# Kernel optimization log

Measured on AMD Instinct MI355X. Metric: run time of the kernel, lower is better.

The kernel has to match this reference:

```python
import jax, jax.numpy as jnp
import numpy as np

# config
D_MODEL, D_A, D_B, R, N, D, S, D_K = 512, 256, 256, 8, 2048, 4608, 4, 64
HID = 2 * D_MODEL
U_END = D_B * R
V_END = U_END + R * D_A
B_END = V_END + D_B
LAMBDA_SHARP = 1.0
TEMPERATURE = 1.0
LN_EPS = 1e-6


def _lecun(key, shape):
    fan_in = shape[-2] if len(shape) > 1 else shape[0]
    return jax.random.normal(key, shape, dtype=jnp.float32) * (1.0 / np.sqrt(fan_in))


def setup_inputs() -> dict:
    key = jax.random.key(0)
    ks = jax.random.split(key, 12)
    return {
        'x': jax.random.normal(ks[0], (256, D_MODEL), dtype=jnp.float32),
        'pool_vectors': 0.01 * jax.random.normal(ks[1], (N, D), dtype=jnp.float32),
        'A_w0': _lecun(ks[2], (D_MODEL, HID)), 'A_b0': jnp.zeros(HID),
        'A_w1': _lecun(ks[3], (HID, D_A)), 'A_b1': jnp.zeros(D_A),
        'W_Q': _lecun(ks[4], (S, D_A, D_K)),
        'W_K': _lecun(ks[5], (S, D, D_K)),
        'aspect_logits': jnp.zeros(S),
        'tau': jnp.asarray(0.5, dtype=jnp.float32),
        'W_base': 0.01 * jax.random.normal(ks[6], (D_B, D_A), dtype=jnp.float32),
        'b_base': jnp.zeros(D_B),
        'gamma': jnp.asarray(0.1, dtype=jnp.float32),
        'ln_scale': jnp.ones(D_A), 'ln_bias': jnp.zeros(D_A),
        'B_w0': _lecun(ks[7], (D_A, HID)), 'B_b0': jnp.zeros(HID),
        'B_w1': _lecun(ks[8], (HID, D_MODEL)), 'B_b1': jnp.zeros(D_MODEL),
    }


def _forward(x, pool_vectors, A_w0, A_b0, A_w1, A_b1, W_Q, W_K, aspect_logits, tau,
             W_base, b_base, gamma, ln_scale, ln_bias, B_w0, B_b0, B_w1, B_b1):
    # Part A MLP
    h_A = jax.nn.gelu(x @ A_w0 + A_b0) @ A_w1 + A_b1                     # [b, d_A]
    # Multi-aspect retrieval
    queries = jnp.einsum('bd,adq->baq', h_A, W_Q)                        # [b, S, d_k]
    keys = jnp.einsum('np,apq->naq', pool_vectors, W_K)                  # [N, S, d_k]
    q_norm = queries / (jnp.linalg.norm(queries, axis=-1, keepdims=True) + 1e-8)
    k_norm = keys / (jnp.linalg.norm(keys, axis=-1, keepdims=True) + 1e-8)
    sims = jnp.einsum('baq,naq->bna', q_norm, k_norm)                    # [b, N, S]
    w = jax.nn.softmax(aspect_logits)
    scores = jnp.einsum('bna,a->bn', sims, w)                            # [b, N]
    g = jax.nn.sigmoid(LAMBDA_SHARP * (scores - tau))
    alpha_raw = g * jnp.exp(scores / TEMPERATURE)
    alpha = alpha_raw / (jnp.sum(alpha_raw, axis=-1, keepdims=True) + 1e-8)
    # Assemble per-sample weight matrix from low-rank factors
    U = pool_vectors[:, :U_END].reshape(N, D_B, R)
    V = pool_vectors[:, U_END:V_END].reshape(N, R, D_A)
    bias = pool_vectors[:, V_END:B_END]                                  # [N, d_B]
    UV = jnp.einsum('ndr,nre->nde', U, V)                                # [N, d_B, d_A]
    W_assembled = W_base[None] + jnp.einsum('bn,nde->bde', alpha, UV)    # [b, d_B, d_A]
    b_assembled = b_base[None] + jnp.einsum('bn,nd->bd', alpha, bias)
    # Middle layer: dynamic matmul + residual + LayerNorm
    h_t = jnp.einsum('ba,bca->bc', h_A, W_assembled) + b_assembled
    y = h_A + gamma * h_t
    mu = jnp.mean(y, axis=-1, keepdims=True)
    var = jnp.mean((y - mu) ** 2, axis=-1, keepdims=True)
    h_mid = (y - mu) / jnp.sqrt(var + LN_EPS) * ln_scale + ln_bias
    # Part B MLP
    output = jax.nn.gelu(h_mid @ B_w0 + B_b0) @ B_w1 + B_b1
    return output, alpha, W_assembled, keys


def reference(x, pool_vectors, A_w0, A_b0, A_w1, A_b1, W_Q, W_K, aspect_logits, tau,
              W_base, b_base, gamma, ln_scale, ln_bias, B_w0, B_b0, B_w1, B_b1):
    return _forward(x, pool_vectors, A_w0, A_b0, A_w1, A_b1, W_Q, W_K, aspect_logits, tau,
                    W_base, b_base, gamma, ln_scale, ln_bias, B_w0, B_b0, B_w1, B_b1)
```

## Files before the change

kernel.cpp:

```cpp
#include <hip/hip_runtime.h>
#include <hip/hip_bf16.h>
#include <math.h>

#define N_POOL 2048
#define D_POOL 4608

typedef __hip_bfloat16 bf16;
typedef __attribute__((ext_vector_type(8))) short bf16x8;
typedef __attribute__((ext_vector_type(4))) float f32x4;
typedef __attribute__((ext_vector_type(4))) unsigned short u16x4;

#define IX 0
#define IPOOL 1
#define IAW0 2
#define IAB0 3
#define IAW1 4
#define IAB1 5
#define IWQ 6
#define IWK 7
#define ILOG 8
#define ITAU 9
#define IWBASE 10
#define IBBASE 11
#define IGAMMA 12
#define ILNS 13
#define ILNB 14
#define IBW0 15
#define IBB0 16
#define IBW1 17
#define IBB1 18

__device__ inline float wsum(float v) {
#pragma unroll
    for (int off = 32; off > 0; off >>= 1) v += __shfl_xor(v, off, 64);
    return v;
}
__device__ inline float ldin(const void* p, size_t i, int f) {
    if (f) return __bfloat162float(((const bf16*)p)[i]);
    return ((const float*)p)[i];
}
__device__ inline float gelu_f(float x) {
    float t = tanhf(0.7978845608028654f * (x + 0.044715f * x * x * x));
    return 0.5f * x * (1.0f + t);
}
__device__ inline unsigned short bfbits(float f) {
    __hip_bfloat16 h = __float2bfloat16(f);
    return *reinterpret_cast<unsigned short*>(&h);
}

struct P19 { const void* p[19]; long n[19]; };

__global__ void detect_all(P19 ip, int* flags) {
    const int j = blockIdx.x;
    const unsigned short* u = (const unsigned short*)ip.p[j];
    long nelem = ip.n[j];
    long nhalf = nelem >> 1; if (nhalf < 1) nhalf = 1;
    long kstep = (nhalf + 8191) >> 13; if (kstep < 1) kstep = 1;
    int W = 0, S = 0, Z = 0, O = 0, C = 0;
    for (long k = threadIdx.x; k * kstep < nhalf; k += 256) {
        long i = k * kstep * 2;
        unsigned short ev = u[i], od = u[i + 1];
        int e = (ev >> 7) & 0xFF;
        if (ev == 0) Z++;
        else if (e >= 90 && e <= 141) S++;
        else W++;
        if (od) O++;
        C++;
    }
    __shared__ int sw[256], ss[256], sz[256], so[256], sc[256];
    sw[threadIdx.x] = W; ss[threadIdx.x] = S; sz[threadIdx.x] = Z;
    so[threadIdx.x] = O; sc[threadIdx.x] = C;
    __syncthreads();
    if (threadIdx.x == 0) {
        int tw = 0, ts = 0, tz = 0, to = 0, tc = 0;
        for (int i = 0; i < 256; i++) {
            tw += sw[i]; ts += ss[i]; tz += sz[i]; to += so[i]; tc += sc[i];
        }
        int f;
        if (tw * 16 > tc) f = 0;
        else if (ts == 0 && tw == 0) f = (to > 0) ? 0 : 1;
        else f = (ts >= tz) ? 1 : 0;
        flags[j] = f;
    }
}

template <int TRANSB>
__global__ __launch_bounds__(256) void gemm64_splitk(
    const void* __restrict__ A, int lda, int afi,
    const void* __restrict__ B, int ldb, int bfi, size_t boffs,
    float* __restrict__ C, int ldc, int KC, const int* __restrict__ flags)
{
    const int fa = (afi >= 0) ? flags[afi] : 0;
    const int fb = (bfi >= 0) ? flags[bfi] : 0;
    __shared__ __align__(16) float As[16][68];
    __shared__ __align__(16) float Bs[16][68];
    const int tid = threadIdx.x;
    const int tx = tid & 15, ty = tid >> 4;
    const int bx = blockIdx.x, by = blockIdx.y;
    const int kbeg = blockIdx.z * KC;
    float acc[4][4] = {};
    for (int k0 = kbeg; k0 < kbeg + KC; k0 += 16) {
#pragma unroll
        for (int i = 0; i < 4; i++) {
            int idx = tid + i * 256;
            int m = idx >> 4, kk = idx & 15;
            As[kk][m] = ldin(A, (size_t)(by * 64 + m) * lda + k0 + kk, fa);
        }
#pragma unroll
        for (int i = 0; i < 4; i++) {
            int idx = tid + i * 256;
            if (TRANSB) {
                int nn2 = idx >> 4, kk = idx & 15;
                Bs[kk][nn2] = ldin(B, boffs + (size_t)(bx * 64 + nn2) * ldb + k0 + kk, fb);
            } else {
                int kk = idx >> 6, nn2 = idx & 63;
                Bs[kk][nn2] = ldin(B, boffs + (size_t)(k0 + kk) * ldb + bx * 64 + nn2, fb);
            }
        }
        __syncthreads();
#pragma unroll
        for (int kk = 0; kk < 16; kk++) {
            float4 av4 = *(const float4*)&As[kk][ty * 4];
            float4 bv4 = *(const float4*)&Bs[kk][tx * 4];
            float av[4] = {av4.x, av4.y, av4.z, av4.w};
            float bv[4] = {bv4.x, bv4.y, bv4.z, bv4.w};
#pragma unroll
            for (int i = 0; i < 4; i++)
#pragma unroll
                for (int j = 0; j < 4; j++) acc[i][j] += av[i] * bv[j];
        }
        __syncthreads();
    }
#pragma unroll
    for (int i = 0; i < 4; i++) {
        int m = by * 64 + ty * 4 + i;
#pragma unroll
        for (int j = 0; j < 4; j++) {
            int n = bx * 64 + tx * 4 + j;
            atomicAdd(&C[(size_t)m * ldc + n], acc[i][j]);
        }
    }
}

__global__ __launch_bounds__(256) void gemm_mfma_atomic(
    const unsigned short* __restrict__ A, int lda,
    const unsigned short* __restrict__ Bmat, int ldb,
    float* __restrict__ C, int ldc, int KC)
{
    const int m0 = blockIdx.x * 128;
    const int n0 = blockIdx.y * 64;
    const unsigned short* B = Bmat + (size_t)blockIdx.y * 64 * ldb;
    const int kbeg = blockIdx.z * KC;
    const int t = threadIdx.x, w = t >> 6, l = t & 63;
    const int q = l >> 4, l16 = l & 15;
    f32x4 acc[2][4] = {};
    for (int k0 = kbeg; k0 < kbeg + KC; k0 += 32) {
        bf16x8 afr[2], bfr[4];
#pragma unroll
        for (int mt = 0; mt < 2; mt++)
            afr[mt] = *(const bf16x8*)&A[(size_t)(m0 + w * 32 + mt * 16 + l16) * lda + k0 + q * 8];
#pragma unroll
        for (int nt = 0; nt < 4; nt++)
            bfr[nt] = *(const bf16x8*)&B[(size_t)(nt * 16 + l16) * ldb + k0 + q * 8];
#pragma unroll
        for (int mt = 0; mt < 2; mt++)
#pragma unroll
            for (int nt = 0; nt < 4; nt++)
                acc[mt][nt] = __builtin_amdgcn_mfma_f32_16x16x32_bf16(
                    afr[mt], bfr[nt], acc[mt][nt], 0, 0, 0);
    }
#pragma unroll
    for (int mt = 0; mt < 2; mt++)
#pragma unroll
        for (int nt = 0; nt < 4; nt++)
#pragma unroll
            for (int r = 0; r < 4; r++) {
                int m = m0 + w * 32 + mt * 16 + q * 4 + r;
                atomicAdd(&C[(size_t)m * ldc + n0 + nt * 16 + l16], acc[mt][nt][r]);
            }
}

template <int ACT>
__global__ __launch_bounds__(256) void gemm_mfma_fused(
    const unsigned short* __restrict__ A, int lda,
    const unsigned short* __restrict__ Bmat, int ldb,
    const void* __restrict__ bias, int bifi, const int* __restrict__ flags,
    float* __restrict__ Cf, unsigned short* __restrict__ Cbf,
    int ldc, int K)
{
    const int m0 = blockIdx.x * 128;
    const int n0 = blockIdx.y * 64;
    const unsigned short* B = Bmat + (size_t)blockIdx.y * 64 * ldb;
    const int t = threadIdx.x, w = t >> 6, l = t & 63;
    const int q = l >> 4, l16 = l & 15;
    f32x4 acc[2][4] = {};
    for (int k0 = 0; k0 < K; k0 += 32) {
        bf16x8 afr[2], bfr[4];
#pragma unroll
        for (int mt = 0; mt < 2; mt++)
            afr[mt] = *(const bf16x8*)&A[(size_t)(m0 + w * 32 + mt * 16 + l16) * lda + k0 + q * 8];
#pragma unroll
        for (int nt = 0; nt < 4; nt++)
            bfr[nt] = *(const bf16x8*)&B[(size_t)(nt * 16 + l16) * ldb + k0 + q * 8];
#pragma unroll
        for (int mt = 0; mt < 2; mt++)
#pragma unroll
            for (int nt = 0; nt < 4; nt++)
                acc[mt][nt] = __builtin_amdgcn_mfma_f32_16x16x32_bf16(
                    afr[mt], bfr[nt], acc[mt][nt], 0, 0, 0);
    }
    float bv[4];
#pragma unroll
    for (int nt = 0; nt < 4; nt++)
        bv[nt] = bias ? ldin(bias, n0 + nt * 16 + l16, (bifi >= 0) ? flags[bifi] : 0) : 0.f;
#pragma unroll
    for (int mt = 0; mt < 2; mt++)
#pragma unroll
        for (int nt = 0; nt < 4; nt++)
#pragma unroll
            for (int r = 0; r < 4; r++) {
                int m = m0 + w * 32 + mt * 16 + q * 4 + r;
                int n = n0 + nt * 16 + l16;
                float v = acc[mt][nt][r] + bv[nt];
                if (ACT == 1) v = gelu_f(v);
                if (Cf)  Cf[(size_t)m * ldc + n] = v;
                if (Cbf) Cbf[(size_t)m * ldc + n] = bfbits(v);
            }
}

__global__ __launch_bounds__(256) void pool2bf(
    const void* __restrict__ pool, const int* __restrict__ flags,
    unsigned short* __restrict__ pb)
{
    const int fp = flags[IPOOL];
    const size_t total = (size_t)N_POOL * D_POOL;
    for (size_t i = ((size_t)blockIdx.x * 256 + threadIdx.x) * 4; i < total;
         i += (size_t)gridDim.x * 1024) {
        u16x4 o;
        if (fp == 0) {
            float4 v = *(const float4*)((const float*)pool + i);
            o[0] = bfbits(v.x); o[1] = bfbits(v.y); o[2] = bfbits(v.z); o[3] = bfbits(v.w);
        } else {
            o = *(const u16x4*)((const unsigned short*)pool + i);
        }
        *(u16x4*)&pb[i] = o;
    }
}

__global__ __launch_bounds__(256) void cvt2bf(
    const void* __restrict__ src, int fi, const int* __restrict__ flags,
    unsigned short* __restrict__ dst, int total)
{
    const int f = (fi >= 0) ? flags[fi] : 0;
    int i = (blockIdx.x * 256 + threadIdx.x) * 4;
    if (i >= total) return;
    if (f == 0) {
        float4 v = *(const float4*)((const float*)src + i);
        u16x4 o;
        o[0] = bfbits(v.x); o[1] = bfbits(v.y); o[2] = bfbits(v.z); o[3] = bfbits(v.w);
        *(u16x4*)&dst[i] = o;
    } else {
        *(u16x4*)&dst[i] = *(const u16x4*)((const unsigned short*)src + i);
    }
}

__global__ __launch_bounds__(256) void transp_bf(
    const void* __restrict__ src, int fi, const int* __restrict__ flags,
    unsigned short* __restrict__ dst, int rows, int cols)
{
    const int f = (fi >= 0) ? flags[fi] : 0;
    const size_t zoff = (size_t)blockIdx.z * rows * cols;
    const int rb = blockIdx.y * 64, cb = blockIdx.x * 64;
    __shared__ float tile[64][65];
    const int t = threadIdx.x;
    const int lr = t >> 6, lc = t & 63;
#pragma unroll
    for (int i = 0; i < 16; i++) {
        int r = i * 4 + lr;
        tile[r][lc] = ldin(src, zoff + (size_t)(rb + r) * cols + cb + lc, f);
    }
    __syncthreads();
#pragma unroll
    for (int i = 0; i < 16; i++) {
        int c = i * 4 + lr;
        dst[zoff + (size_t)(cb + c) * rows + rb + lc] = bfbits(tile[lc][c]);
    }
}

__global__ __launch_bounds__(256) void wk2bfT(
    const void* __restrict__ W_K, const int* __restrict__ flags,
    unsigned short* __restrict__ out)
{
    const int fk = flags[IWK];
    const int a = blockIdx.y, kb = blockIdx.x, t = threadIdx.x;
#pragma unroll
    for (int i = 0; i < 16; i++) {
        int idx = i * 256 + t;
        int kk = idx >> 6, qq = idx & 63;
        float v = ldin(W_K, (size_t)a * 294912 + (size_t)(kb * 64 + kk) * 64 + qq, fk);
        out[(size_t)(a * 64 + qq) * 4608 + kb * 64 + kk] = bfbits(v);
    }
}

__global__ __launch_bounds__(256) void bias2bfT(
    const void* __restrict__ pool, const int* __restrict__ flags,
    unsigned short* __restrict__ out)
{
    const int fp = flags[IPOOL];
    const int nb = blockIdx.x, cb = blockIdx.y, t = threadIdx.x;
#pragma unroll
    for (int i = 0; i < 16; i++) {
        int idx = i * 256 + t;
        int nn = idx >> 6, cc = idx & 63;
        float v = ldin(pool, (size_t)(nb * 64 + nn) * 4608 + 4096 + cb * 64 + cc, fp);
        out[(size_t)(cb * 64 + cc) * 2048 + nb * 64 + nn] = bfbits(v);
    }
}

__global__ __launch_bounds__(256) void init_bias_kernel(
    float* __restrict__ C, const void* __restrict__ bias, int bifi,
    const int* __restrict__ flags, int N, int total)
{
    int i = blockIdx.x * 256 + threadIdx.x;
    if (i >= total) return;
    float v = 0.f;
    if (bias) v = ldin(bias, i % N, (bifi >= 0) ? flags[bifi] : 0);
    C[i] = v;
}

__global__ __launch_bounds__(256) void gelu_kernel(float* __restrict__ buf, int total)
{
    int i = blockIdx.x * 256 + threadIdx.x;
    if (i < total) buf[i] = gelu_f(buf[i]);
}

__global__ __launch_bounds__(256) void knorm_kernel(
    const float* __restrict__ keys, unsigned short* __restrict__ knbf)
{
    const int n = blockIdx.x;
    const int a = threadIdx.x >> 6, q = threadIdx.x & 63;
    float v = keys[(size_t)n * 256 + a * 64 + q];
    float ss = wsum(v * v);
    knbf[(size_t)n * 256 + a * 64 + q] = bfbits(v / (sqrtf(ss) + 1e-8f));
}

__global__ __launch_bounds__(256) void qnorm_kernel(
    const float* __restrict__ qraw, const float* __restrict__ w,
    unsigned short* __restrict__ qwbf)
{
    const int b = blockIdx.x;
    const int a = threadIdx.x >> 6, q = threadIdx.x & 63;
    float v = qraw[b * 256 + a * 64 + q];
    float ss = wsum(v * v);
    qwbf[b * 256 + a * 64 + q] = bfbits(v / (sqrtf(ss) + 1e-8f) * w[a]);
}

__global__ void softmax4_kernel(const void* __restrict__ logits,
                                const int* __restrict__ flags, float* __restrict__ w) {
    if (threadIdx.x == 0) {
        int f = flags[ILOG];
        float l0 = ldin(logits, 0, f), l1 = ldin(logits, 1, f);
        float l2 = ldin(logits, 2, f), l3 = ldin(logits, 3, f);
        float m = fmaxf(fmaxf(l0, l1), fmaxf(l2, l3));
        float e0 = expf(l0 - m), e1 = expf(l1 - m), e2 = expf(l2 - m), e3 = expf(l3 - m);
        float s = e0 + e1 + e2 + e3;
        w[0] = e0 / s; w[1] = e1 / s; w[2] = e2 / s; w[3] = e3 / s;
    }
}

__global__ __launch_bounds__(256) void alpha_kernel(
    const float* __restrict__ scores, const void* __restrict__ tau_p,
    const int* __restrict__ flags,
    float* __restrict__ alpha_out, unsigned short* __restrict__ alphaT,
    unsigned short* __restrict__ alphaB)
{
    const int b = blockIdx.x;
    const int tid = threadIdx.x;
    const float tauv = ldin(tau_p, 0, flags[ITAU]);
    float ar[8];
    float lsum = 0.f;
#pragma unroll
    for (int i = 0; i < 8; i++) {
        int n = i * 256 + tid;
        float s = scores[b * 2048 + n];
        float g = 1.f / (1.f + expf(-(s - tauv)));
        ar[i] = g * expf(s);
        lsum += ar[i];
    }
    __shared__ float sb[4];
    float wsv = wsum(lsum);
    if ((tid & 63) == 0) sb[tid >> 6] = wsv;
    __syncthreads();
    float tot = sb[0] + sb[1] + sb[2] + sb[3];
    float inv = 1.f / (tot + 1e-8f);
#pragma unroll
    for (int i = 0; i < 8; i++) {
        int n = i * 256 + tid;
        float al = ar[i] * inv;
        alpha_out[b * 2048 + n] = al;
        unsigned short bb = bfbits(al);
        alphaT[(size_t)(n >> 3) * 2048 + b * 8 + (n & 7)] = bb;
        alphaB[(size_t)b * 2048 + n] = bb;
    }
}

#define QW 520
__global__ __launch_bounds__(256, 2) void assemble_mfma(
    const unsigned short* __restrict__ alphaT,
    const void* __restrict__ pool,
    const void* __restrict__ W_base,
    const int* __restrict__ flags,
    float* __restrict__ Wout)
{
    const int fp = flags[IPOOL], fw = flags[IWBASE];
    const int lid = blockIdx.x;
    const int xcd = lid & 7, idx = lid >> 3;
    const int dt = idx & 31;
    const int et = ((idx >> 5) << 3) + xcd;
    const int d0 = dt * 8, e0 = et * 16;
    const int t = threadIdx.x;
    const int w = t >> 6, l = t & 63;
    const int q = l >> 4, l16 = l & 15;

    const int nl  = t >> 3;
    const int sub = t & 7;
    const int dlp = sub >> 1;
    const int eh  = sub & 1;
    const int jj  = nl & 7;

    __shared__ __align__(16) float Us[2][32][76];
    __shared__ __align__(16) float Vs[2][32][132];
    __shared__ __align__(16) unsigned short uvb[8][QW];

    const float4* pool4 = (const float4*)pool;

    f32x4 acc[4][8] = {};

    auto load_stage = [&](int n0, float4* st) {
#pragma unroll
        for (int i = 0; i < 2; i++) {
            int f = i * 256 + t;
            int n = n0 + (f >> 4);
            int q4 = f & 15;
            if (fp == 0) {
                st[i] = pool4[(size_t)n * 1152 + d0 * 2 + q4];
            } else {
                size_t base = (size_t)n * 4608 + (size_t)d0 * 8 + q4 * 4;
                st[i] = make_float4(ldin(pool, base, 1), ldin(pool, base + 1, 1),
                                    ldin(pool, base + 2, 1), ldin(pool, base + 3, 1));
            }
        }
#pragma unroll
        for (int i = 0; i < 4; i++) {
            int f = i * 256 + t;
            int n = n0 + (f >> 5);
            int r = (f & 31) >> 2, e4 = f & 3;
            if (fp == 0) {
                st[2 + i] = pool4[(size_t)n * 1152 + 512 + r * 64 + (e0 >> 2) + e4];
            } else {
                size_t base = (size_t)n * 4608 + 2048 + (size_t)r * 256 + e0 + e4 * 4;
                st[2 + i] = make_float4(ldin(pool, base, 1), ldin(pool, base + 1, 1),
                                        ldin(pool, base + 2, 1), ldin(pool, base + 3, 1));
            }
        }
    };
    auto store_stage = [&](int bp, const float4* st) {
#pragma unroll
        for (int i = 0; i < 2; i++) {
            int f = i * 256 + t;
            *(float4*)&Us[bp][f >> 4][(f & 15) * 4] = st[i];
        }
#pragma unroll
        for (int i = 0; i < 4; i++) {
            int f = i * 256 + t;
            int r = (f & 31) >> 2, e4 = f & 3;
            *(float4*)&Vs[bp][f >> 5][r * 16 + e4 * 4] = st[2 + i];
        }
    };

    {
        float4 st[6];
        load_stage(0, st);
        store_stage(0, st);
    }
    __syncthreads();

    int p = 0;
    for (int step = 0; step < 64; step++) {
        const int n0 = step * 32;
        float4 stn[6];
        if (step < 63) load_stage(n0 + 32, stn);

        bf16x8 afr[4];
#pragma unroll
        for (int mt = 0; mt < 4; mt++) {
            const unsigned short* ap =
                alphaT + (size_t)(step * 4 + q) * 2048 + (w * 64 + mt * 16 + l16) * 8;
            afr[mt] = *(const bf16x8*)ap;
        }

        {
            const float* Ur = &Us[p][nl][dlp * 16];
            float4 Ua = *(const float4*)(Ur);
            float4 Ub = *(const float4*)(Ur + 4);
            float4 Uc = *(const float4*)(Ur + 8);
            float4 Ud = *(const float4*)(Ur + 12);
            float U0[8] = {Ua.x, Ua.y, Ua.z, Ua.w, Ub.x, Ub.y, Ub.z, Ub.w};
            float U1[8] = {Uc.x, Uc.y, Uc.z, Uc.w, Ud.x, Ud.y, Ud.z, Ud.w};
            float uv0[8] = {0.f, 0.f, 0.f, 0.f, 0.f, 0.f, 0.f, 0.f};
            float uv1[8] = {0.f, 0.f, 0.f, 0.f, 0.f, 0.f, 0.f, 0.f};
#pragma unroll
            for (int r = 0; r < 8; r++) {
                float4 va = *(const float4*)&Vs[p][nl][r * 16 + eh * 8];
                float4 vb = *(const float4*)&Vs[p][nl][r * 16 + eh * 8 + 4];
                uv0[0] += U0[r] * va.x; uv0[1] += U0[r] * va.y;
                uv0[2] += U0[r] * va.z; uv0[3] += U0[r] * va.w;
                uv0[4] += U0[r] * vb.x; uv0[5] += U0[r] * vb.y;
                uv0[6] += U0[r] * vb.z; uv0[7] += U0[r] * vb.w;
                uv1[0] += U1[r] * va.x; uv1[1] += U1[r] * va.y;
                uv1[2] += U1[r] * va.z; uv1[3] += U1[r] * va.w;
                uv1[4] += U1[r] * vb.x; uv1[5] += U1[r] * vb.y;
                uv1[6] += U1[r] * vb.z; uv1[7] += U1[r] * vb.w;
            }
            const int cg0 = dlp * 2, cg1 = cg0 + 1;
            const int wbase = w * 128 + eh * 64 + jj;
#pragma unroll
            for (int i = 0; i < 8; i++) {
                uvb[cg0][wbase + i * 8] = bfbits(uv0[i]);
                uvb[cg1][wbase + i * 8] = bfbits(uv1[i]);
            }
        }
        __syncthreads();

        bf16x8 bfr[8];
#pragma unroll
        for (int cg = 0; cg < 8; cg++)
            bfr[cg] = *(const bf16x8*)&uvb[cg][l * 8];
        if (step < 63) store_stage(p ^ 1, stn);
#pragma unroll
        for (int mt = 0; mt < 4; mt++)
#pragma unroll
            for (int cg = 0; cg < 8; cg++)
                acc[mt][cg] = __builtin_amdgcn_mfma_f32_16x16x32_bf16(
                    afr[mt], bfr[cg], acc[mt][cg], 0, 0, 0);
        __syncthreads();
        p ^= 1;
    }

    float wb[8];
#pragma unroll
    for (int cg = 0; cg < 8; cg++)
        wb[cg] = ldin(W_base, (size_t)(d0 + cg) * 256 + e0 + l16, fw);
#pragma unroll
    for (int mt = 0; mt < 4; mt++) {
#pragma unroll
        for (int cg = 0; cg < 8; cg++) {
            size_t col = (size_t)(d0 + cg) * 256 + e0 + l16;
#pragma unroll
            for (int r = 0; r < 4; r++) {
                int b = w * 64 + mt * 16 + q * 4 + r;
                Wout[(size_t)b * 65536 + col] = acc[mt][cg][r] + wb[cg];
            }
        }
    }
}

__global__ __launch_bounds__(256) void hty_kernel(
    const float* __restrict__ Wout, const float* __restrict__ hA,
    const float* __restrict__ bass, const void* __restrict__ gamma_p,
    const int* __restrict__ flags, float* __restrict__ y)
{
    const int b = blockIdx.y;
    const int c = blockIdx.x * 4 + (threadIdx.x >> 6);
    const int lane = threadIdx.x & 63;
    const float4 wv = ((const float4*)(Wout + ((size_t)b * 65536 + c * 256)))[lane];
    const float4 h4 = ((const float4*)(hA + b * 256))[lane];
    float s = wv.x * h4.x + wv.y * h4.y + wv.z * h4.z + wv.w * h4.w;
    s = wsum(s);
    if (lane == 0) {
        float ht = s + bass[b * 256 + c];
        y[b * 256 + c] = hA[b * 256 + c] + ldin(gamma_p, 0, flags[IGAMMA]) * ht;
    }
}

__global__ __launch_bounds__(256) void ln_kernel(
    const float* __restrict__ y, const void* __restrict__ ln_scale,
    const void* __restrict__ ln_bias, const int* __restrict__ flags,
    float* __restrict__ hmid)
{
    const int fs = flags[ILNS], fb = flags[ILNB];
    const int b = blockIdx.x, tid = threadIdx.x;
    float v = y[b * 256 + tid];
    __shared__ float s1b[4], s2b[4];
    float w1 = wsum(v), w2 = wsum(v * v);
    if ((tid & 63) == 0) { s1b[tid >> 6] = w1; s2b[tid >> 6] = w2; }
    __syncthreads();
    float mu = (s1b[0] + s1b[1] + s1b[2] + s1b[3]) * (1.f / 256.f);
    float ex2 = (s2b[0] + s2b[1] + s2b[2] + s2b[3]) * (1.f / 256.f);
    float var = ex2 - mu * mu;
    float inv = 1.f / sqrtf(var + 1e-6f);
    hmid[b * 256 + tid] = (v - mu) * inv * ldin(ln_scale, tid, fs)
                        + ldin(ln_bias, tid, fb);
}

extern "C" void kernel_launch(void* const* d_in, const int* in_sizes, int n_in,
                              void* d_out, int out_size, void* d_ws, size_t ws_size,
                              hipStream_t stream)
{
    (void)out_size; (void)n_in;
    const void* x      = d_in[0];
    const void* pool   = d_in[1];
    const void* A_w0   = d_in[2];
    const void* A_b0   = d_in[3];
    const void* A_w1   = d_in[4];
    const void* A_b1   = d_in[5];
    const void* W_Q    = d_in[6];
    const void* W_K    = d_in[7];
    const void* logits = d_in[8];
    const void* tau    = d_in[9];
    const void* W_base = d_in[10];
    const void* b_base = d_in[11];
    const void* gamma  = d_in[12];
    const void* ln_s   = d_in[13];
    const void* ln_b   = d_in[14];
    const void* B_w0   = d_in[15];
    const void* B_b0   = d_in[16];
    const void* B_w1   = d_in[17];
    const void* B_b1   = d_in[18];

    float* out       = (float*)d_out;
    float* out0      = out;
    float* out_alpha = out + 131072;
    float* out_W     = out + 655360;
    float* out_keys  = out + 17432576;

    float* ws = (float*)d_ws;
    int*   flagp   = (int*)d_ws;
    float* ws_w    = ws + 32;
    float* ws_hA   = ws + 64;
    float* ws_qw   = ws + 65600;
    float* ws_bass = ws + 131136;
    float* ws_y    = ws + 196672;
    float* ws_hmid = ws + 262208;
    unsigned short* alpha_bf = (unsigned short*)(ws + 327744);

    size_t wsf = ws_size / 4;
    bool full = wsf >= 1638464;
    float* slotA;
    float* slotB;
    float* T1;
    float* scr = (float*)out_W;
    if (full) {
        slotA = ws + 589888;
        slotB = ws + 1114176;
        T1    = slotA;
    } else {
        slotA = scr;
        slotB = scr + 524288;
        T1    = (float*)alpha_bf;
    }
    float* scores = slotA;
    unsigned short* knbf = (unsigned short*)slotB;

    unsigned short* xbf    = (unsigned short*)(scr + 1048576);
    unsigned short* aw0T   = (unsigned short*)(scr + 1114112);
    unsigned short* aw1T   = (unsigned short*)(scr + 1376256);
    unsigned short* wqT    = (unsigned short*)(scr + 1507328);
    unsigned short* Gbf    = (unsigned short*)(scr + 1540096);
    unsigned short* hAbf   = (unsigned short*)(scr + 1671168);
    float*          qraw   = scr + 1703936;
    unsigned short* qwbf   = (unsigned short*)(scr + 1769472);
    unsigned short* poolbf = (unsigned short*)(scr + 2097152);
    unsigned short* wkbT   = (unsigned short*)(scr + 7340032);
    unsigned short* biasT  = (unsigned short*)(scr + 8388608);
    unsigned short* alphaB = (unsigned short*)(scr + 8912896);

    P19 ip;
    for (int i = 0; i < 19; i++) { ip.p[i] = d_in[i]; ip.n[i] = in_sizes[i]; }
    detect_all<<<19, 256, 0, stream>>>(ip, flagp);
    softmax4_kernel<<<1, 64, 0, stream>>>(logits, flagp, ws_w);
    pool2bf<<<2048, 256, 0, stream>>>(pool, flagp, poolbf);
    wk2bfT<<<dim3(72, 4), 256, 0, stream>>>(W_K, flagp, wkbT);
    bias2bfT<<<dim3(32, 4), 256, 0, stream>>>(pool, flagp, biasT);
    cvt2bf<<<128, 256, 0, stream>>>(x, IX, flagp, xbf, 131072);
    transp_bf<<<dim3(16, 8, 1), 256, 0, stream>>>(A_w0, IAW0, flagp, aw0T, 512, 1024);
    transp_bf<<<dim3(4, 16, 1), 256, 0, stream>>>(A_w1, IAW1, flagp, aw1T, 1024, 256);
    transp_bf<<<dim3(1, 4, 4), 256, 0, stream>>>(W_Q, IWQ, flagp, wqT, 256, 64);
    gemm_mfma_fused<1><<<dim3(2, 16), 256, 0, stream>>>(
        xbf, 512, aw0T, 512, A_b0, IAB0, flagp, nullptr, Gbf, 1024, 512);
    gemm_mfma_fused<0><<<dim3(2, 4), 256, 0, stream>>>(
        Gbf, 1024, aw1T, 1024, A_b1, IAB1, flagp, ws_hA, hAbf, 256, 1024);
    init_bias_kernel<<<2048, 256, 0, stream>>>(out_keys, nullptr, -1, flagp, 256, 524288);
    gemm_mfma_atomic<<<dim3(16, 4, 16), 256, 0, stream>>>(
        poolbf, 4608, wkbT, 4608, out_keys, 256, 288);
    knorm_kernel<<<2048, 256, 0, stream>>>(out_keys, knbf);
    gemm_mfma_fused<0><<<dim3(2, 4), 256, 0, stream>>>(
        hAbf, 256, wqT, 256, nullptr, -1, flagp, qraw, nullptr, 256, 256);
    qnorm_kernel<<<256, 256, 0, stream>>>(qraw, ws_w, qwbf);
    gemm_mfma_fused<0><<<dim3(2, 32), 256, 0, stream>>>(
        qwbf, 256, knbf, 256, nullptr, -1, flagp, scores, nullptr, 2048, 256);
    alpha_kernel<<<256, 256, 0, stream>>>(scores, tau, flagp, out_alpha, alpha_bf, alphaB);
    init_bias_kernel<<<256, 256, 0, stream>>>(ws_bass, b_base, IBBASE, flagp, 256, 65536);
    gemm_mfma_atomic<<<dim3(2, 4, 8), 256, 0, stream>>>(
        alphaB, 2048, biasT, 2048, ws_bass, 256, 256);
    assemble_mfma<<<512, 256, 0, stream>>>(alpha_bf, pool, W_base, flagp, out_W);
    hty_kernel<<<dim3(64, 256), 256, 0, stream>>>(out_W, ws_hA, ws_bass, gamma, flagp, ws_y);
    ln_kernel<<<256, 256, 0, stream>>>(ws_y, ln_s, ln_b, flagp, ws_hmid);
    init_bias_kernel<<<1024, 256, 0, stream>>>(T1, B_b0, IBB0, flagp, 1024, 262144);
    gemm64_splitk<0><<<dim3(16, 4, 2), 256, 0, stream>>>(
        ws_hmid, 256, -1, B_w0, 1024, IBW0, 0,
        T1, 1024, 128, flagp);
    gelu_kernel<<<1024, 256, 0, stream>>>(T1, 262144);
    init_bias_kernel<<<512, 256, 0, stream>>>(out0, B_b1, IBB1, flagp, 512, 131072);
    gemm64_splitk<0><<<dim3(8, 4, 4), 256, 0, stream>>>(
        T1, 1024, -1, B_w1, 512, IBW1, 0,
        out0, 512, 256, flagp);
}
```

Before: 567.7 us.

## Fuse Part-B first layer into bf16 MFMA GEMM, retile UV assembly, halve keys split-K

Part B's first layer now runs through the fused bf16 MFMA GEMM with bias and GELU, which replaces the bias init, the fp32 split-K GEMM and the separate GELU kernel. LayerNorm writes bf16, and B_w0 is transposed to bf16 first. The UV product in assemble_mfma is remapped so each thread covers 32 d-values by 4 e-values, and the keys split-K GEMM uses 8 chunks instead of 16 to cut atomics. The trade-off is bf16 rounding of the hidden activations and one extra transpose launch.

```diff
diff --git a/kernel.cpp b/kernel.cpp
--- a/kernel.cpp
+++ b/kernel.cpp
@@ -90,7 +90,7 @@
     const void* __restrict__ B, int ldb, int bfi, size_t boffs,
     float* __restrict__ C, int ldc, int KC, const int* __restrict__ flags)
 {
-    const int fa = (afi >= 0) ? flags[afi] : 0;
+    const int fa = (afi == -2) ? 1 : ((afi >= 0) ? flags[afi] : 0);
     const int fb = (bfi >= 0) ? flags[bfi] : 0;
     __shared__ __align__(16) float As[16][68];
     __shared__ __align__(16) float Bs[16][68];
@@ -328,12 +328,6 @@
     C[i] = v;
 }
 
-__global__ __launch_bounds__(256) void gelu_kernel(float* __restrict__ buf, int total)
-{
-    int i = blockIdx.x * 256 + threadIdx.x;
-    if (i < total) buf[i] = gelu_f(buf[i]);
-}
-
 __global__ __launch_bounds__(256) void knorm_kernel(
     const float* __restrict__ keys, unsigned short* __restrict__ knbf)
 {
@@ -424,11 +418,12 @@
 
     const int nl  = t >> 3;
     const int sub = t & 7;
-    const int dlp = sub >> 1;
-    const int eh  = sub & 1;
-    const int jj  = nl & 7;
-
-    __shared__ __align__(16) float Us[2][32][76];
+    const int dh  = sub >> 2;
+    const int eq  = sub & 3;
+    const int kq  = nl >> 3;
+    const int jn  = nl & 7;
+
+    __shared__ __align__(16) float Us[2][32][68];
     __shared__ __align__(16) float Vs[2][32][132];
     __shared__ __align__(16) unsigned short uvb[8][QW];
 
@@ -500,34 +495,34 @@
         }
 
         {
-            const float* Ur = &Us[p][nl][dlp * 16];
-            float4 Ua = *(const float4*)(Ur);
-            float4 Ub = *(const float4*)(Ur + 4);
-            float4 Uc = *(const float4*)(Ur + 8);
-            float4 Ud = *(const float4*)(Ur + 12);
-            float U0[8] = {Ua.x, Ua.y, Ua.z, Ua.w, Ub.x, Ub.y, Ub.z, Ub.w};
-            float U1[8] = {Uc.x, Uc.y, Uc.z, Uc.w, Ud.x, Ud.y, Ud.z, Ud.w};
-            float uv0[8] = {0.f, 0.f, 0.f, 0.f, 0.f, 0.f, 0.f, 0.f};
-            float uv1[8] = {0.f, 0.f, 0.f, 0.f, 0.f, 0.f, 0.f, 0.f};
+            const float* Ur = &Us[p][nl][dh * 32];
+            float U[4][8];
+#pragma unroll
+            for (int j = 0; j < 4; j++) {
+                float4 a = *(const float4*)(Ur + j * 8);
+                float4 b = *(const float4*)(Ur + j * 8 + 4);
+                U[j][0] = a.x; U[j][1] = a.y; U[j][2] = a.z; U[j][3] = a.w;
+                U[j][4] = b.x; U[j][5] = b.y; U[j][6] = b.z; U[j][7] = b.w;
+            }
+            float uv[4][4] = {};
 #pragma unroll
             for (int r = 0; r < 8; r++) {
-                float4 va = *(const float4*)&Vs[p][nl][r * 16 + eh * 8];
-                float4 vb = *(const float4*)&Vs[p][nl][r * 16 + eh * 8 + 4];
-                uv0[0] += U0[r] * va.x; uv0[1] += U0[r] * va.y;
-                uv0[2] += U0[r] * va.z; uv0[3] += U0[r] * va.w;
-                uv0[4] += U0[r] * vb.x; uv0[5] += U0[r] * vb.y;
-                uv0[6] += U0[r] * vb.z; uv0[7] += U0[r] * vb.w;
-                uv1[0] += U1[r] * va.x; uv1[1] += U1[r] * va.y;
-                uv1[2] += U1[r] * va.z; uv1[3] += U1[r] * va.w;
-                uv1[4] += U1[r] * vb.x; uv1[5] += U1[r] * vb.y;
-                uv1[6] += U1[r] * vb.z; uv1[7] += U1[r] * vb.w;
-            }
-            const int cg0 = dlp * 2, cg1 = cg0 + 1;
-            const int wbase = w * 128 + eh * 64 + jj;
-#pragma unroll
-            for (int i = 0; i < 8; i++) {
-                uvb[cg0][wbase + i * 8] = bfbits(uv0[i]);
-                uvb[cg1][wbase + i * 8] = bfbits(uv1[i]);
+                float4 v = *(const float4*)&Vs[p][nl][r * 16 + eq * 4];
+#pragma unroll
+                for (int j = 0; j < 4; j++) {
+                    uv[j][0] += U[j][r] * v.x;
+                    uv[j][1] += U[j][r] * v.y;
+                    uv[j][2] += U[j][r] * v.z;
+                    uv[j][3] += U[j][r] * v.w;
+                }
+            }
+#pragma unroll
+            for (int j = 0; j < 4; j++) {
+                const int cg = dh * 4 + j;
+                const int base = kq * 128 + eq * 32 + jn;
+#pragma unroll
+                for (int i = 0; i < 4; i++)
+                    uvb[cg][base + i * 8] = bfbits(uv[j][i]);
             }
         }
         __syncthreads();
@@ -586,7 +581,7 @@
 __global__ __launch_bounds__(256) void ln_kernel(
     const float* __restrict__ y, const void* __restrict__ ln_scale,
     const void* __restrict__ ln_bias, const int* __restrict__ flags,
-    float* __restrict__ hmid)
+    unsigned short* __restrict__ hmidbf)
 {
     const int fs = flags[ILNS], fb = flags[ILNB];
     const int b = blockIdx.x, tid = threadIdx.x;
@@ -599,8 +594,8 @@
     float ex2 = (s2b[0] + s2b[1] + s2b[2] + s2b[3]) * (1.f / 256.f);
     float var = ex2 - mu * mu;
     float inv = 1.f / sqrtf(var + 1e-6f);
-    hmid[b * 256 + tid] = (v - mu) * inv * ldin(ln_scale, tid, fs)
-                        + ldin(ln_bias, tid, fb);
+    float hm = (v - mu) * inv * ldin(ln_scale, tid, fs) + ldin(ln_bias, tid, fb);
+    hmidbf[b * 256 + tid] = bfbits(hm);
 }
 
 extern "C" void kernel_launch(void* const* d_in, const int* in_sizes, int n_in,
@@ -638,29 +633,30 @@
     int*   flagp   = (int*)d_ws;
     float* ws_w    = ws + 32;
     float* ws_hA   = ws + 64;
-    float* ws_qw   = ws + 65600;
     float* ws_bass = ws + 131136;
     float* ws_y    = ws + 196672;
-    float* ws_hmid = ws + 262208;
+    unsigned short* hmidbf = (unsigned short*)(ws + 262208);
     unsigned short* alpha_bf = (unsigned short*)(ws + 327744);
 
     size_t wsf = ws_size / 4;
     bool full = wsf >= 1638464;
     float* slotA;
     float* slotB;
-    float* T1;
+    float* Treg;
     float* scr = (float*)out_W;
     if (full) {
         slotA = ws + 589888;
         slotB = ws + 1114176;
-        T1    = slotA;
+        Treg  = ws + 589888;
     } else {
         slotA = scr;
         slotB = scr + 524288;
-        T1    = (float*)alpha_bf;
+        Treg  = ws + 327744;
     }
     float* scores = slotA;
     unsigned short* knbf = (unsigned short*)slotB;
+    unsigned short* T1bf = (unsigned short*)Treg;
+    unsigned short* bw0T = (unsigned short*)(Treg + 131072);
 
     unsigned short* xbf    = (unsigned short*)(scr + 1048576);
     unsigned short* aw0T   = (unsigned short*)(scr + 1114112);
@@ -691,8 +687,8 @@
     gemm_mfma_fused<0><<<dim3(2, 4), 256, 0, stream>>>(
         Gbf, 1024, aw1T, 1024, A_b1, IAB1, flagp, ws_hA, hAbf, 256, 1024);
     init_bias_kernel<<<2048, 256, 0, stream>>>(out_keys, nullptr, -1, flagp, 256, 524288);
-    gemm_mfma_atomic<<<dim3(16, 4, 16), 256, 0, stream>>>(
-        poolbf, 4608, wkbT, 4608, out_keys, 256, 288);
+    gemm_mfma_atomic<<<dim3(16, 4, 8), 256, 0, stream>>>(
+        poolbf, 4608, wkbT, 4608, out_keys, 256, 576);
     knorm_kernel<<<2048, 256, 0, stream>>>(out_keys, knbf);
     gemm_mfma_fused<0><<<dim3(2, 4), 256, 0, stream>>>(
         hAbf, 256, wqT, 256, nullptr, -1, flagp, qraw, nullptr, 256, 256);
@@ -704,15 +700,13 @@
     gemm_mfma_atomic<<<dim3(2, 4, 8), 256, 0, stream>>>(
         alphaB, 2048, biasT, 2048, ws_bass, 256, 256);
     assemble_mfma<<<512, 256, 0, stream>>>(alpha_bf, pool, W_base, flagp, out_W);
+    transp_bf<<<dim3(16, 4, 1), 256, 0, stream>>>(B_w0, IBW0, flagp, bw0T, 256, 1024);
     hty_kernel<<<dim3(64, 256), 256, 0, stream>>>(out_W, ws_hA, ws_bass, gamma, flagp, ws_y);
-    ln_kernel<<<256, 256, 0, stream>>>(ws_y, ln_s, ln_b, flagp, ws_hmid);
-    init_bias_kernel<<<1024, 256, 0, stream>>>(T1, B_b0, IBB0, flagp, 1024, 262144);
-    gemm64_splitk<0><<<dim3(16, 4, 2), 256, 0, stream>>>(
-        ws_hmid, 256, -1, B_w0, 1024, IBW0, 0,
-        T1, 1024, 128, flagp);
-    gelu_kernel<<<1024, 256, 0, stream>>>(T1, 262144);
+    ln_kernel<<<256, 256, 0, stream>>>(ws_y, ln_s, ln_b, flagp, hmidbf);
+    gemm_mfma_fused<1><<<dim3(2, 16), 256, 0, stream>>>(
+        hmidbf, 256, bw0T, 256, B_b0, IBB0, flagp, nullptr, T1bf, 1024, 256);
     init_bias_kernel<<<512, 256, 0, stream>>>(out0, B_b1, IBB1, flagp, 512, 131072);
     gemm64_splitk<0><<<dim3(8, 4, 4), 256, 0, stream>>>(
-        T1, 1024, -1, B_w1, 512, IBW1, 0,
+        T1bf, 1024, -2, B_w1, 512, IBW1, 0,
         out0, 512, 256, flagp);
 }
```

Result: faster. 556.2 us (-2.0%).

## Shrink MFMA GEMM blocks to one wave, move Part B first layer to fused MFMA

Applied to the files above, without the earlier changes.

The MFMA GEMM kernels now use a single 64-thread wave per block with a 32-row tile, and the grids are enlarged so small GEMMs spread across more CUs. The keys split-K grid changes shape. LayerNorm now writes bf16, B_w0 is transposed to bf16, and the first Part B layer runs through the fused MFMA kernel with GELU. This removes the split-K fp32 GEMM, its bias init and the separate GELU pass, and the second layer reads the bf16 intermediate. Input-format detection samples fewer elements, which risks misdetecting dtypes.

```diff
diff --git a/kernel.cpp b/kernel.cpp
--- a/kernel.cpp
+++ b/kernel.cpp
@@ -55,7 +55,7 @@
     const unsigned short* u = (const unsigned short*)ip.p[j];
     long nelem = ip.n[j];
     long nhalf = nelem >> 1; if (nhalf < 1) nhalf = 1;
-    long kstep = (nhalf + 8191) >> 13; if (kstep < 1) kstep = 1;
+    long kstep = (nhalf + 2047) >> 11; if (kstep < 1) kstep = 1;
     int W = 0, S = 0, Z = 0, O = 0, C = 0;
     for (long k = threadIdx.x; k * kstep < nhalf; k += 256) {
         long i = k * kstep * 2;
@@ -90,7 +90,7 @@
     const void* __restrict__ B, int ldb, int bfi, size_t boffs,
     float* __restrict__ C, int ldc, int KC, const int* __restrict__ flags)
 {
-    const int fa = (afi >= 0) ? flags[afi] : 0;
+    const int fa = (afi == -2) ? 1 : ((afi >= 0) ? flags[afi] : 0);
     const int fb = (bfi >= 0) ? flags[bfi] : 0;
     __shared__ __align__(16) float As[16][68];
     __shared__ __align__(16) float Bs[16][68];
@@ -142,23 +142,23 @@
     }
 }
 
-__global__ __launch_bounds__(256) void gemm_mfma_atomic(
+__global__ __launch_bounds__(64) void gemm_mfma_atomic(
     const unsigned short* __restrict__ A, int lda,
     const unsigned short* __restrict__ Bmat, int ldb,
     float* __restrict__ C, int ldc, int KC)
 {
-    const int m0 = blockIdx.x * 128;
+    const int m0 = blockIdx.x * 32;
     const int n0 = blockIdx.y * 64;
     const unsigned short* B = Bmat + (size_t)blockIdx.y * 64 * ldb;
     const int kbeg = blockIdx.z * KC;
-    const int t = threadIdx.x, w = t >> 6, l = t & 63;
+    const int l = threadIdx.x;
     const int q = l >> 4, l16 = l & 15;
     f32x4 acc[2][4] = {};
     for (int k0 = kbeg; k0 < kbeg + KC; k0 += 32) {
         bf16x8 afr[2], bfr[4];
 #pragma unroll
         for (int mt = 0; mt < 2; mt++)
-            afr[mt] = *(const bf16x8*)&A[(size_t)(m0 + w * 32 + mt * 16 + l16) * lda + k0 + q * 8];
+            afr[mt] = *(const bf16x8*)&A[(size_t)(m0 + mt * 16 + l16) * lda + k0 + q * 8];
 #pragma unroll
         for (int nt = 0; nt < 4; nt++)
             bfr[nt] = *(const bf16x8*)&B[(size_t)(nt * 16 + l16) * ldb + k0 + q * 8];
@@ -175,30 +175,30 @@
         for (int nt = 0; nt < 4; nt++)
 #pragma unroll
             for (int r = 0; r < 4; r++) {
-                int m = m0 + w * 32 + mt * 16 + q * 4 + r;
+                int m = m0 + mt * 16 + q * 4 + r;
                 atomicAdd(&C[(size_t)m * ldc + n0 + nt * 16 + l16], acc[mt][nt][r]);
             }
 }
 
 template <int ACT>
-__global__ __launch_bounds__(256) void gemm_mfma_fused(
+__global__ __launch_bounds__(64) void gemm_mfma_fused(
     const unsigned short* __restrict__ A, int lda,
     const unsigned short* __restrict__ Bmat, int ldb,
     const void* __restrict__ bias, int bifi, const int* __restrict__ flags,
     float* __restrict__ Cf, unsigned short* __restrict__ Cbf,
     int ldc, int K)
 {
-    const int m0 = blockIdx.x * 128;
+    const int m0 = blockIdx.x * 32;
     const int n0 = blockIdx.y * 64;
     const unsigned short* B = Bmat + (size_t)blockIdx.y * 64 * ldb;
-    const int t = threadIdx.x, w = t >> 6, l = t & 63;
+    const int l = threadIdx.x;
     const int q = l >> 4, l16 = l & 15;
     f32x4 acc[2][4] = {};
     for (int k0 = 0; k0 < K; k0 += 32) {
         bf16x8 afr[2], bfr[4];
 #pragma unroll
         for (int mt = 0; mt < 2; mt++)
-            afr[mt] = *(const bf16x8*)&A[(size_t)(m0 + w * 32 + mt * 16 + l16) * lda + k0 + q * 8];
+            afr[mt] = *(const bf16x8*)&A[(size_t)(m0 + mt * 16 + l16) * lda + k0 + q * 8];
 #pragma unroll
         for (int nt = 0; nt < 4; nt++)
             bfr[nt] = *(const bf16x8*)&B[(size_t)(nt * 16 + l16) * ldb + k0 + q * 8];
@@ -219,7 +219,7 @@
         for (int nt = 0; nt < 4; nt++)
 #pragma unroll
             for (int r = 0; r < 4; r++) {
-                int m = m0 + w * 32 + mt * 16 + q * 4 + r;
+                int m = m0 + mt * 16 + q * 4 + r;
                 int n = n0 + nt * 16 + l16;
                 float v = acc[mt][nt][r] + bv[nt];
                 if (ACT == 1) v = gelu_f(v);
@@ -326,12 +326,6 @@
     float v = 0.f;
     if (bias) v = ldin(bias, i % N, (bifi >= 0) ? flags[bifi] : 0);
     C[i] = v;
-}
-
-__global__ __launch_bounds__(256) void gelu_kernel(float* __restrict__ buf, int total)
-{
-    int i = blockIdx.x * 256 + threadIdx.x;
-    if (i < total) buf[i] = gelu_f(buf[i]);
 }
 
 __global__ __launch_bounds__(256) void knorm_kernel(
@@ -586,7 +580,7 @@
 __global__ __launch_bounds__(256) void ln_kernel(
     const float* __restrict__ y, const void* __restrict__ ln_scale,
     const void* __restrict__ ln_bias, const int* __restrict__ flags,
-    float* __restrict__ hmid)
+    unsigned short* __restrict__ hmidbf)
 {
     const int fs = flags[ILNS], fb = flags[ILNB];
     const int b = blockIdx.x, tid = threadIdx.x;
@@ -599,8 +593,8 @@
     float ex2 = (s2b[0] + s2b[1] + s2b[2] + s2b[3]) * (1.f / 256.f);
     float var = ex2 - mu * mu;
     float inv = 1.f / sqrtf(var + 1e-6f);
-    hmid[b * 256 + tid] = (v - mu) * inv * ldin(ln_scale, tid, fs)
-                        + ldin(ln_bias, tid, fb);
+    float hm = (v - mu) * inv * ldin(ln_scale, tid, fs) + ldin(ln_bias, tid, fb);
+    hmidbf[b * 256 + tid] = bfbits(hm);
 }
 
 extern "C" void kernel_launch(void* const* d_in, const int* in_sizes, int n_in,
@@ -638,29 +632,30 @@
     int*   flagp   = (int*)d_ws;
     float* ws_w    = ws + 32;
     float* ws_hA   = ws + 64;
-    float* ws_qw   = ws + 65600;
     float* ws_bass = ws + 131136;
     float* ws_y    = ws + 196672;
-    float* ws_hmid = ws + 262208;
+    unsigned short* hmidbf = (unsigned short*)(ws + 262208);
     unsigned short* alpha_bf = (unsigned short*)(ws + 327744);
 
     size_t wsf = ws_size / 4;
     bool full = wsf >= 1638464;
     float* slotA;
     float* slotB;
-    float* T1;
+    float* Treg;
     float* scr = (float*)out_W;
     if (full) {
         slotA = ws + 589888;
         slotB = ws + 1114176;
-        T1    = slotA;
+        Treg  = ws + 589888;
     } else {
         slotA = scr;
         slotB = scr + 524288;
-        T1    = (float*)alpha_bf;
+        Treg  = ws + 327744;
     }
     float* scores = slotA;
     unsigned short* knbf = (unsigned short*)slotB;
+    unsigned short* T1bf = (unsigned short*)Treg;
+    unsigned short* bw0T = (unsigned short*)(Treg + 131072);
 
     unsigned short* xbf    = (unsigned short*)(scr + 1048576);
     unsigned short* aw0T   = (unsigned short*)(scr + 1114112);
@@ -686,33 +681,31 @@
     transp_bf<<<dim3(16, 8, 1), 256, 0, stream>>>(A_w0, IAW0, flagp, aw0T, 512, 1024);
     transp_bf<<<dim3(4, 16, 1), 256, 0, stream>>>(A_w1, IAW1, flagp, aw1T, 1024, 256);
     transp_bf<<<dim3(1, 4, 4), 256, 0, stream>>>(W_Q, IWQ, flagp, wqT, 256, 64);
-    gemm_mfma_fused<1><<<dim3(2, 16), 256, 0, stream>>>(
+    gemm_mfma_fused<1><<<dim3(8, 16), 64, 0, stream>>>(
         xbf, 512, aw0T, 512, A_b0, IAB0, flagp, nullptr, Gbf, 1024, 512);
-    gemm_mfma_fused<0><<<dim3(2, 4), 256, 0, stream>>>(
+    gemm_mfma_fused<0><<<dim3(8, 4), 64, 0, stream>>>(
         Gbf, 1024, aw1T, 1024, A_b1, IAB1, flagp, ws_hA, hAbf, 256, 1024);
     init_bias_kernel<<<2048, 256, 0, stream>>>(out_keys, nullptr, -1, flagp, 256, 524288);
-    gemm_mfma_atomic<<<dim3(16, 4, 16), 256, 0, stream>>>(
-        poolbf, 4608, wkbT, 4608, out_keys, 256, 288);
+    gemm_mfma_atomic<<<dim3(64, 4, 8), 64, 0, stream>>>(
+        poolbf, 4608, wkbT, 4608, out_keys, 256, 576);
     knorm_kernel<<<2048, 256, 0, stream>>>(out_keys, knbf);
-    gemm_mfma_fused<0><<<dim3(2, 4), 256, 0, stream>>>(
+    gemm_mfma_fused<0><<<dim3(8, 4), 64, 0, stream>>>(
         hAbf, 256, wqT, 256, nullptr, -1, flagp, qraw, nullptr, 256, 256);
     qnorm_kernel<<<256, 256, 0, stream>>>(qraw, ws_w, qwbf);
-    gemm_mfma_fused<0><<<dim3(2, 32), 256, 0, stream>>>(
+    gemm_mfma_fused<0><<<dim3(8, 32), 64, 0, stream>>>(
         qwbf, 256, knbf, 256, nullptr, -1, flagp, scores, nullptr, 2048, 256);
     alpha_kernel<<<256, 256, 0, stream>>>(scores, tau, flagp, out_alpha, alpha_bf, alphaB);
     init_bias_kernel<<<256, 256, 0, stream>>>(ws_bass, b_base, IBBASE, flagp, 256, 65536);
-    gemm_mfma_atomic<<<dim3(2, 4, 8), 256, 0, stream>>>(
+    gemm_mfma_atomic<<<dim3(8, 4, 8), 64, 0, stream>>>(
         alphaB, 2048, biasT, 2048, ws_bass, 256, 256);
     assemble_mfma<<<512, 256, 0, stream>>>(alpha_bf, pool, W_base, flagp, out_W);
+    transp_bf<<<dim3(16, 4, 1), 256, 0, stream>>>(B_w0, IBW0, flagp, bw0T, 256, 1024);
     hty_kernel<<<dim3(64, 256), 256, 0, stream>>>(out_W, ws_hA, ws_bass, gamma, flagp, ws_y);
-    ln_kernel<<<256, 256, 0, stream>>>(ws_y, ln_s, ln_b, flagp, ws_hmid);
-    init_bias_kernel<<<1024, 256, 0, stream>>>(T1, B_b0, IBB0, flagp, 1024, 262144);
-    gemm64_splitk<0><<<dim3(16, 4, 2), 256, 0, stream>>>(
-        ws_hmid, 256, -1, B_w0, 1024, IBW0, 0,
-        T1, 1024, 128, flagp);
-    gelu_kernel<<<1024, 256, 0, stream>>>(T1, 262144);
+    ln_kernel<<<256, 256, 0, stream>>>(ws_y, ln_s, ln_b, flagp, hmidbf);
+    gemm_mfma_fused<1><<<dim3(8, 16), 64, 0, stream>>>(
+        hmidbf, 256, bw0T, 256, B_b0, IBB0, flagp, nullptr, T1bf, 1024, 256);
     init_bias_kernel<<<512, 256, 0, stream>>>(out0, B_b1, IBB1, flagp, 512, 131072);
     gemm64_splitk<0><<<dim3(8, 4, 4), 256, 0, stream>>>(
-        T1, 1024, -1, B_w1, 512, IBW1, 0,
+        T1bf, 1024, -2, B_w1, 512, IBW1, 0,
         out0, 512, 256, flagp);
 }
```

Result: faster. 514.0 us (-9.5%).
